# Kernel tuning notes

Measured on AMD Instinct MI355X. Metric: run time of the kernel, lower is better.

The kernel has to match this reference:

```python
import jax, jax.numpy as jnp
import numpy as np

NEG_SLOPE = 0.2  # LeakyReLU negative slope (act_negative)


def setup_inputs() -> dict:
    key = jax.random.key(0)
    ks = jax.random.split(key, 5)
    B, N, D = 64, 4096, 16
    x = jax.random.normal(ks[0], (B, N, D), dtype=jnp.float32)
    # random adjacency, scaled so row sums are O(1) and activations stay stable
    adj = jax.random.uniform(ks[1], (N, N), dtype=jnp.float32) * (2.0 / N)
    Identity = jnp.eye(N, dtype=jnp.float32)
    W0 = jax.random.normal(ks[2], (D, D), dtype=jnp.float32) * (1.0 / np.sqrt(D))
    W1 = jax.random.normal(ks[3], (D, D), dtype=jnp.float32) * (1.0 / np.sqrt(D))
    W2 = jax.random.normal(ks[4], (D, D), dtype=jnp.float32) * (1.0 / np.sqrt(D))
    return {"x": x, "adj": adj, "Identity": Identity, "W0": W0, "W1": W1, "W2": W2}


def _gcn_layer(x, W, adj, I):
    # GCNConv: linear (no bias) -> leaky_relu -> batched adjacency matmul.
    # The same conv (same W) is applied with adj and with Identity, then summed.
    h = jax.nn.leaky_relu(jnp.einsum('bnd,de->bne', x, W), NEG_SLOPE)
    out_adj = jnp.einsum('nm,bmh->bnh', adj, h)  # replaces per-sample torch.mm loop
    out_id = jnp.einsum('nm,bmh->bnh', I, h)
    return out_adj + out_id


def reference(x, adj, Identity, W0, W1, W2):
    out = _gcn_layer(x, W0, adj, Identity)
    out = _gcn_layer(out, W1, adj, Identity)
    out = _gcn_layer(out, W2, adj, Identity)
    return out  # is_residual=False: no shortcut branch
```

## Files before the change

### kernel.cpp

```cpp
#include <hip/hip_runtime.h>
#include <stdint.h>


typedef float  f32x4  __attribute__((ext_vector_type(4)));
typedef unsigned short ushort8 __attribute__((ext_vector_type(8)));
typedef int    i32x4  __attribute__((ext_vector_type(4)));
typedef int    i32x8  __attribute__((ext_vector_type(8)));

typedef __attribute__((address_space(1))) void* as1p;
typedef __attribute__((address_space(3))) void* as3p;
#define GLOAD_LDS16(G, L) \
  __builtin_amdgcn_global_load_lds((as1p)(G), (as3p)(L), 16, 0, 0)

#define P_ELEMS 4194304
#define ADJ_SCALE 4096.0f
#define ADJ_DESCALE (1.0f / 4096.0f)
#define SCALE_ONE 0x7f7f7f7f

__device__ __forceinline__ unsigned short f2bf(float f) {
  unsigned u = __float_as_uint(f);
  u += 0x7fffu + ((u >> 16) & 1u);
  return (unsigned short)(u >> 16);
}
__device__ __forceinline__ float bf2f(unsigned short u) {
  return __uint_as_float(((unsigned)u) << 16);
}
__device__ __forceinline__ int pk4_fp8(float a, float b, float c, float d) {
  int v = __builtin_amdgcn_cvt_pk_fp8_f32(a, b, 0, false);
  v = __builtin_amdgcn_cvt_pk_fp8_f32(c, d, v, true);
  return v;
}

__global__ void prep(const float* __restrict__ adj,
                     unsigned char* __restrict__ a8,
                     const float* __restrict__ x,
                     const float* __restrict__ W,
                     unsigned char* __restrict__ hb8,
                     unsigned short* __restrict__ hnc_out) {
  __shared__ float xs[64 * 65];
  __shared__ unsigned short ht[64 * 72];
  int bid = blockIdx.x;

  if (bid >= 1024) {
    size_t base = ((size_t)(bid - 1024) * 256 + threadIdx.x) * 16;
    const float4* src = (const float4*)(adj + base);
    float4 q0 = src[0], q1 = src[1], q2 = src[2], q3 = src[3];
    int4 o;
    o.x = pk4_fp8(q0.x * ADJ_SCALE, q0.y * ADJ_SCALE, q0.z * ADJ_SCALE, q0.w * ADJ_SCALE);
    o.y = pk4_fp8(q1.x * ADJ_SCALE, q1.y * ADJ_SCALE, q1.z * ADJ_SCALE, q1.w * ADJ_SCALE);
    o.z = pk4_fp8(q2.x * ADJ_SCALE, q2.y * ADJ_SCALE, q2.z * ADJ_SCALE, q2.w * ADJ_SCALE);
    o.w = pk4_fp8(q3.x * ADJ_SCALE, q3.y * ADJ_SCALE, q3.z * ADJ_SCALE, q3.w * ADJ_SCALE);
    *(int4*)(a8 + base) = o;
    return;
  }

  int n0 = (bid & 63) * 64, c0 = (bid >> 6) * 64;

  for (int i = threadIdx.x; i < 1024; i += 256) {
    int bs = i >> 8, rem = i & 255, nr = rem >> 2, d4 = rem & 3;
    float4 v = *(const float4*)(
        x + ((size_t)(c0 / 16 + bs) * 4096 + n0 + nr) * 16 + d4 * 4);
    float* dst = xs + nr * 65 + bs * 16 + d4 * 4;
    dst[0] = v.x; dst[1] = v.y; dst[2] = v.z; dst[3] = v.w;
  }
  __syncthreads();

  int n_l = threadIdx.x & 63, b_l = threadIdx.x >> 6;
  float xv[16];
#pragma unroll
  for (int d = 0; d < 16; ++d) xv[d] = xs[n_l * 65 + b_l * 16 + d];
  float accv[16];
#pragma unroll
  for (int e = 0; e < 16; ++e) accv[e] = 0.f;
#pragma unroll
  for (int d = 0; d < 16; ++d)
#pragma unroll
    for (int e = 0; e < 16; ++e) accv[e] += xv[d] * W[d * 16 + e];

  ushort8 h0, h1;
#pragma unroll
  for (int e = 0; e < 16; ++e) {
    float a = accv[e] > 0.f ? accv[e] : 0.2f * accv[e];
    unsigned short hv = f2bf(a);
    ht[(b_l * 16 + e) * 72 + n_l] = hv;
    if (e < 8) h0[e] = hv; else h1[e - 8] = hv;
  }
  unsigned short* ho = hnc_out + (size_t)(n0 + n_l) * 1024 + c0 + b_l * 16;
  *(ushort8*)(ho)     = h0;
  *(ushort8*)(ho + 8) = h1;
  __syncthreads();

  for (int i = threadIdx.x; i < 512; i += 256) {
    int row = i >> 3, ch = i & 7;
    const unsigned short* s = ht + row * 72 + ch * 8;
    int2 v;
    v.x = pk4_fp8(bf2f(s[0]), bf2f(s[1]), bf2f(s[2]), bf2f(s[3]));
    v.y = pk4_fp8(bf2f(s[4]), bf2f(s[5]), bf2f(s[6]), bf2f(s[7]));
    *(int2*)(hb8 + (size_t)(c0 + row) * 4096 + n0 + ch * 8) = v;
  }
}

__global__ void linear_fuse(const unsigned short* __restrict__ pp,
                            const unsigned short* __restrict__ hnc_in,
                            const float* __restrict__ W,
                            unsigned char* __restrict__ hb8,
                            unsigned short* __restrict__ hnc_out) {
  __shared__ float xs[64 * 65];
  __shared__ unsigned short ht[64 * 72];
  int n0 = blockIdx.x * 64, c0 = blockIdx.y * 64;

  for (int i = threadIdx.x; i < 512; i += 256) {
    int row = i >> 3, ch = i & 7;
    size_t g = (size_t)(n0 + row) * 1024 + c0 + ch * 8;
    ushort8 a = *(const ushort8*)(pp + g);
    ushort8 b = *(const ushort8*)(pp + P_ELEMS + g);
    ushort8 c = *(const ushort8*)(hnc_in + g);
    float* dst = xs + row * 65 + ch * 8;
#pragma unroll
    for (int j = 0; j < 8; ++j) dst[j] = bf2f(a[j]) + bf2f(b[j]) + bf2f(c[j]);
  }
  __syncthreads();

  int n_l = threadIdx.x & 63, b_l = threadIdx.x >> 6;
  float xv[16];
#pragma unroll
  for (int d = 0; d < 16; ++d) xv[d] = xs[n_l * 65 + b_l * 16 + d];
  float accv[16];
#pragma unroll
  for (int e = 0; e < 16; ++e) accv[e] = 0.f;
#pragma unroll
  for (int d = 0; d < 16; ++d)
#pragma unroll
    for (int e = 0; e < 16; ++e) accv[e] += xv[d] * W[d * 16 + e];

  ushort8 h0, h1;
#pragma unroll
  for (int e = 0; e < 16; ++e) {
    float a = accv[e] > 0.f ? accv[e] : 0.2f * accv[e];
    unsigned short hv = f2bf(a);
    ht[(b_l * 16 + e) * 72 + n_l] = hv;
    if (e < 8) h0[e] = hv; else h1[e - 8] = hv;
  }
  unsigned short* ho = hnc_out + (size_t)(n0 + n_l) * 1024 + c0 + b_l * 16;
  *(ushort8*)(ho)     = h0;
  *(ushort8*)(ho + 8) = h1;
  __syncthreads();

  for (int i = threadIdx.x; i < 512; i += 256) {
    int row = i >> 3, ch = i & 7;
    const unsigned short* s = ht + row * 72 + ch * 8;
    int2 v;
    v.x = pk4_fp8(bf2f(s[0]), bf2f(s[1]), bf2f(s[2]), bf2f(s[3]));
    v.y = pk4_fp8(bf2f(s[4]), bf2f(s[5]), bf2f(s[6]), bf2f(s[7]));
    *(int2*)(hb8 + (size_t)(c0 + row) * 4096 + n0 + ch * 8) = v;
  }
}

__global__ void add_out(const unsigned short* __restrict__ pp,
                        const unsigned short* __restrict__ hnc,
                        float* __restrict__ out) {
  int gid = blockIdx.x * 256 + threadIdx.x;
  int n = gid >> 7, c8 = (gid & 127) * 8;
  size_t g = (size_t)n * 1024 + c8;
  ushort8 a = *(const ushort8*)(pp + g);
  ushort8 b = *(const ushort8*)(pp + P_ELEMS + g);
  ushort8 h = *(const ushort8*)(hnc + g);
  float v[8];
#pragma unroll
  for (int j = 0; j < 8; ++j) v[j] = bf2f(a[j]) + bf2f(b[j]) + bf2f(h[j]);
  int bb = c8 >> 4, d0 = c8 & 15;
  float* o = out + (size_t)bb * 65536 + n * 16 + d0;
  *(float4*)(o)     = float4{v[0], v[1], v[2], v[3]};
  *(float4*)(o + 4) = float4{v[4], v[5], v[6], v[7]};
}

__global__ __launch_bounds__(256, 2)
void gemm_f8(const unsigned char* __restrict__ A,
             const unsigned char* __restrict__ B8,
             unsigned short* __restrict__ pp) {
  const int K = 4096;
  __shared__ unsigned char a_s[2][128 * 128];
  __shared__ unsigned char b_s[2][128 * 128];

  int tid = threadIdx.x, wave = tid >> 6, lane = tid & 63;

  int lin = blockIdx.x;
  int xcd = lin & 7, g = lin >> 3;
  int mth = g & 3, ct = (g >> 2) & 7, ks = g >> 5;
  int mt = mth * 8 + xcd;
  int n0 = mt * 128, c0 = ct * 128;
  int kbase = ks * 2048;

  int l8 = lane >> 3, lc = lane & 7;
  int swc = lc ^ l8;
  const unsigned char* gA[4];
  const unsigned char* gB[4];
#pragma unroll
  for (int j = 0; j < 4; ++j) {
    int r = wave * 32 + j * 8 + l8;
    gA[j] = A  + (size_t)(n0 + r) * K + kbase + swc * 16;
    gB[j] = B8 + (size_t)(c0 + r) * K + kbase + swc * 16;
  }

  int i16 = lane & 15, q = lane >> 4;
  int wm = wave >> 1, wn = wave & 1;
  int sw7 = i16 & 7;
  int pc0 = ((2 * q) ^ sw7) * 16;
  int pc1 = ((2 * q + 1) ^ sw7) * 16;

#define STAGE(buf, k0)                                                \
  do {                                                                \
    _Pragma("unroll")                                                 \
    for (int j = 0; j < 4; ++j) {                                     \
      GLOAD_LDS16(gA[j] + (k0), a_s[buf] + (wave * 32 + j * 8) * 128);\
      GLOAD_LDS16(gB[j] + (k0), b_s[buf] + (wave * 32 + j * 8) * 128);\
    }                                                                 \
  } while (0)

#define COMPUTE(buf)                                                  \
  do {                                                                \
    i32x8 bv[4];                                                      \
    _Pragma("unroll")                                                 \
    for (int u = 0; u < 4; ++u) {                                     \
      const unsigned char* bp = b_s[buf] + (wn * 64 + u * 16 + i16) * 128; \
      i32x4 blo = *(const i32x4*)(bp + pc0);                          \
      i32x4 bhi = *(const i32x4*)(bp + pc1);                          \
      bv[u] = __builtin_shufflevector(blo, bhi, 0, 1, 2, 3, 4, 5, 6, 7); \
    }                                                                 \
    _Pragma("unroll")                                                 \
    for (int t = 0; t < 4; ++t) {                                     \
      const unsigned char* ap = a_s[buf] + (wm * 64 + t * 16 + i16) * 128; \
      i32x4 alo = *(const i32x4*)(ap + pc0);                          \
      i32x4 ahi = *(const i32x4*)(ap + pc1);                          \
      i32x8 av = __builtin_shufflevector(alo, ahi, 0, 1, 2, 3, 4, 5, 6, 7); \
      _Pragma("unroll")                                               \
      for (int u = 0; u < 4; ++u)                                     \
        acc[t][u] = __builtin_amdgcn_mfma_scale_f32_16x16x128_f8f6f4( \
            av, bv[u], acc[t][u], 0, 0, 0, SCALE_ONE, 0, SCALE_ONE);  \
    }                                                                 \
  } while (0)

  f32x4 acc[4][4] = {};

  STAGE(0, 0);
  __syncthreads();

  for (int it = 0; it < 16; it += 2) {
    STAGE(1, (it + 1) * 128);
    COMPUTE(0);
    __syncthreads();

    if (it + 2 < 16) STAGE(0, (it + 2) * 128);
    COMPUTE(1);
    __syncthreads();
  }

#undef STAGE
#undef COMPUTE

  unsigned short* dst = pp + (size_t)ks * P_ELEMS;
#pragma unroll
  for (int t = 0; t < 4; ++t)
#pragma unroll
    for (int u = 0; u < 4; ++u)
#pragma unroll
      for (int i = 0; i < 4; ++i) {
        int n_g = n0 + wm * 64 + t * 16 + q * 4 + i;
        int c_g = c0 + wn * 64 + u * 16 + i16;
        dst[(size_t)n_g * 1024 + c_g] = f2bf(acc[t][u][i] * ADJ_DESCALE);
      }
}

extern "C" void kernel_launch(void* const* d_in, const int* in_sizes, int n_in,
                              void* d_out, int out_size, void* d_ws, size_t ws_size,
                              hipStream_t stream) {
  const float* x   = (const float*)d_in[0];
  const float* adj = (const float*)d_in[1];
  const float* W0  = (const float*)d_in[3];
  const float* W1  = (const float*)d_in[4];
  const float* W2  = (const float*)d_in[5];
  float* out = (float*)d_out;

  char* ws = (char*)d_ws;
  unsigned char*  adj8 = (unsigned char*)ws;
  unsigned char*  hb8  = (unsigned char*)(ws + 16777216);
  unsigned short* hnc  = (unsigned short*)(ws + 20971520);
  unsigned short* pp   = (unsigned short*)(ws + 29360128);

  prep<<<5120, 256, 0, stream>>>(adj, adj8, x, W0, hb8, hnc);
  gemm_f8<<<512, 256, 0, stream>>>(adj8, hb8, pp);
  linear_fuse<<<dim3(64, 16), 256, 0, stream>>>(pp, hnc, W1, hb8, hnc);
  gemm_f8<<<512, 256, 0, stream>>>(adj8, hb8, pp);
  linear_fuse<<<dim3(64, 16), 256, 0, stream>>>(pp, hnc, W2, hb8, hnc);
  gemm_f8<<<512, 256, 0, stream>>>(adj8, hb8, pp);
  add_out<<<2048, 256, 0, stream>>>(pp, hnc, out);
}
```

Baseline: 246.9 us.

## Fuse linear+activation epilogue into FP8 GEMM, drop split-K, triple-buffer LDS

Removes the split-K partial buffers and the separate linear_fuse/add_out kernels by doing the full K reduction in one block and running the residual add, 16x16 linear, LeakyReLU and FP8 transposed repack in the GEMM epilogue through LDS. The main loop moves to a three-stage global_load_lds pipeline with explicit vmcnt waits and barriers, and occupancy is lowered to one block per CU. This saves the partial-sum write/read traffic and kernel launches but halves the grid to 256 blocks with a longer K loop, which risks underfilling the CUs. Ping-pong hb8 buffers avoid read/write hazards across layers.

Measured after the change: 261.7 us. 1.06x slower.

```diff
diff --git a/kernel.cpp b/kernel.cpp
--- a/kernel.cpp
+++ b/kernel.cpp
@@ -12,7 +12,6 @@
 #define GLOAD_LDS16(G, L) \
   __builtin_amdgcn_global_load_lds((as1p)(G), (as3p)(L), 16, 0, 0)
 
-#define P_ELEMS 4194304
 #define ADJ_SCALE 4096.0f
 #define ADJ_DESCALE (1.0f / 4096.0f)
 #define SCALE_ONE 0x7f7f7f7f
@@ -100,96 +99,26 @@
   }
 }
 
-__global__ void linear_fuse(const unsigned short* __restrict__ pp,
-                            const unsigned short* __restrict__ hnc_in,
-                            const float* __restrict__ W,
-                            unsigned char* __restrict__ hb8,
-                            unsigned short* __restrict__ hnc_out) {
-  __shared__ float xs[64 * 65];
-  __shared__ unsigned short ht[64 * 72];
-  int n0 = blockIdx.x * 64, c0 = blockIdx.y * 64;
-
-  for (int i = threadIdx.x; i < 512; i += 256) {
-    int row = i >> 3, ch = i & 7;
-    size_t g = (size_t)(n0 + row) * 1024 + c0 + ch * 8;
-    ushort8 a = *(const ushort8*)(pp + g);
-    ushort8 b = *(const ushort8*)(pp + P_ELEMS + g);
-    ushort8 c = *(const ushort8*)(hnc_in + g);
-    float* dst = xs + row * 65 + ch * 8;
-#pragma unroll
-    for (int j = 0; j < 8; ++j) dst[j] = bf2f(a[j]) + bf2f(b[j]) + bf2f(c[j]);
-  }
-  __syncthreads();
-
-  int n_l = threadIdx.x & 63, b_l = threadIdx.x >> 6;
-  float xv[16];
-#pragma unroll
-  for (int d = 0; d < 16; ++d) xv[d] = xs[n_l * 65 + b_l * 16 + d];
-  float accv[16];
-#pragma unroll
-  for (int e = 0; e < 16; ++e) accv[e] = 0.f;
-#pragma unroll
-  for (int d = 0; d < 16; ++d)
-#pragma unroll
-    for (int e = 0; e < 16; ++e) accv[e] += xv[d] * W[d * 16 + e];
-
-  ushort8 h0, h1;
-#pragma unroll
-  for (int e = 0; e < 16; ++e) {
-    float a = accv[e] > 0.f ? accv[e] : 0.2f * accv[e];
-    unsigned short hv = f2bf(a);
-    ht[(b_l * 16 + e) * 72 + n_l] = hv;
-    if (e < 8) h0[e] = hv; else h1[e - 8] = hv;
-  }
-  unsigned short* ho = hnc_out + (size_t)(n0 + n_l) * 1024 + c0 + b_l * 16;
-  *(ushort8*)(ho)     = h0;
-  *(ushort8*)(ho + 8) = h1;
-  __syncthreads();
-
-  for (int i = threadIdx.x; i < 512; i += 256) {
-    int row = i >> 3, ch = i & 7;
-    const unsigned short* s = ht + row * 72 + ch * 8;
-    int2 v;
-    v.x = pk4_fp8(bf2f(s[0]), bf2f(s[1]), bf2f(s[2]), bf2f(s[3]));
-    v.y = pk4_fp8(bf2f(s[4]), bf2f(s[5]), bf2f(s[6]), bf2f(s[7]));
-    *(int2*)(hb8 + (size_t)(c0 + row) * 4096 + n0 + ch * 8) = v;
-  }
-}
-
-__global__ void add_out(const unsigned short* __restrict__ pp,
-                        const unsigned short* __restrict__ hnc,
-                        float* __restrict__ out) {
-  int gid = blockIdx.x * 256 + threadIdx.x;
-  int n = gid >> 7, c8 = (gid & 127) * 8;
-  size_t g = (size_t)n * 1024 + c8;
-  ushort8 a = *(const ushort8*)(pp + g);
-  ushort8 b = *(const ushort8*)(pp + P_ELEMS + g);
-  ushort8 h = *(const ushort8*)(hnc + g);
-  float v[8];
-#pragma unroll
-  for (int j = 0; j < 8; ++j) v[j] = bf2f(a[j]) + bf2f(b[j]) + bf2f(h[j]);
-  int bb = c8 >> 4, d0 = c8 & 15;
-  float* o = out + (size_t)bb * 65536 + n * 16 + d0;
-  *(float4*)(o)     = float4{v[0], v[1], v[2], v[3]};
-  *(float4*)(o + 4) = float4{v[4], v[5], v[6], v[7]};
-}
-
-__global__ __launch_bounds__(256, 2)
+__global__ __launch_bounds__(256, 1)
 void gemm_f8(const unsigned char* __restrict__ A,
              const unsigned char* __restrict__ B8,
-             unsigned short* __restrict__ pp) {
+             const float* __restrict__ Wn,
+             unsigned short* __restrict__ hnc,
+             unsigned char* __restrict__ hb8o,
+             float* __restrict__ out,
+             int mode) {
   const int K = 4096;
-  __shared__ unsigned char a_s[2][128 * 128];
-  __shared__ unsigned char b_s[2][128 * 128];
+  __shared__ unsigned char smem[98304];
+  unsigned char* a_s[3] = {smem, smem + 16384, smem + 32768};
+  unsigned char* b_s[3] = {smem + 49152, smem + 65536, smem + 81920};
 
   int tid = threadIdx.x, wave = tid >> 6, lane = tid & 63;
 
   int lin = blockIdx.x;
   int xcd = lin & 7, g = lin >> 3;
-  int mth = g & 3, ct = (g >> 2) & 7, ks = g >> 5;
+  int mth = g & 3, ct = g >> 2;
   int mt = mth * 8 + xcd;
   int n0 = mt * 128, c0 = ct * 128;
-  int kbase = ks * 2048;
 
   int l8 = lane >> 3, lc = lane & 7;
   int swc = lc ^ l8;
@@ -198,8 +127,8 @@
 #pragma unroll
   for (int j = 0; j < 4; ++j) {
     int r = wave * 32 + j * 8 + l8;
-    gA[j] = A  + (size_t)(n0 + r) * K + kbase + swc * 16;
-    gB[j] = B8 + (size_t)(c0 + r) * K + kbase + swc * 16;
+    gA[j] = A  + (size_t)(n0 + r) * K + swc * 16;
+    gB[j] = B8 + (size_t)(c0 + r) * K + swc * 16;
   }
 
   int i16 = lane & 15, q = lane >> 4;
@@ -208,12 +137,13 @@
   int pc0 = ((2 * q) ^ sw7) * 16;
   int pc1 = ((2 * q + 1) ^ sw7) * 16;
 
-#define STAGE(buf, k0)                                                \
+#define STAGE(buf, it)                                                \
   do {                                                                \
+    int k0_ = (it) * 128;                                             \
     _Pragma("unroll")                                                 \
     for (int j = 0; j < 4; ++j) {                                     \
-      GLOAD_LDS16(gA[j] + (k0), a_s[buf] + (wave * 32 + j * 8) * 128);\
-      GLOAD_LDS16(gB[j] + (k0), b_s[buf] + (wave * 32 + j * 8) * 128);\
+      GLOAD_LDS16(gA[j] + k0_, a_s[buf] + (wave * 32 + j * 8) * 128); \
+      GLOAD_LDS16(gB[j] + k0_, b_s[buf] + (wave * 32 + j * 8) * 128); \
     }                                                                 \
   } while (0)
 
@@ -240,35 +170,113 @@
     }                                                                 \
   } while (0)
 
+#define WAITVM8() asm volatile("s_waitcnt vmcnt(8)" ::: "memory")
+#define WAITVM0() asm volatile("s_waitcnt vmcnt(0)" ::: "memory")
+#define BARX() do { __builtin_amdgcn_s_barrier(); \
+                    asm volatile("" ::: "memory"); } while (0)
+
   f32x4 acc[4][4] = {};
 
   STAGE(0, 0);
-  __syncthreads();
-
-  for (int it = 0; it < 16; it += 2) {
-    STAGE(1, (it + 1) * 128);
-    COMPUTE(0);
-    __syncthreads();
-
-    if (it + 2 < 16) STAGE(0, (it + 2) * 128);
-    COMPUTE(1);
-    __syncthreads();
-  }
+  STAGE(1, 1);
+
+  for (int itb = 0; itb < 30; itb += 3) {
+    WAITVM8(); BARX(); STAGE(2, itb + 2); COMPUTE(0);
+    WAITVM8(); BARX(); STAGE(0, itb + 3); COMPUTE(1);
+    WAITVM8(); BARX(); STAGE(1, itb + 4); COMPUTE(2);
+  }
+  WAITVM8(); BARX(); COMPUTE(0);
+  WAITVM0(); BARX(); COMPUTE(1);
 
 #undef STAGE
 #undef COMPUTE
-
-  unsigned short* dst = pp + (size_t)ks * P_ELEMS;
+#undef WAITVM8
+#undef WAITVM0
+#undef BARX
+
+  __syncthreads();
+  float* u_lds = (float*)smem;
+  unsigned short* ht = (unsigned short*)(smem + 65536);
+
 #pragma unroll
   for (int t = 0; t < 4; ++t)
 #pragma unroll
     for (int u = 0; u < 4; ++u)
 #pragma unroll
       for (int i = 0; i < 4; ++i) {
-        int n_g = n0 + wm * 64 + t * 16 + q * 4 + i;
-        int c_g = c0 + wn * 64 + u * 16 + i16;
-        dst[(size_t)n_g * 1024 + c_g] = f2bf(acc[t][u][i] * ADJ_DESCALE);
+        int n_l = wm * 64 + t * 16 + q * 4 + i;
+        int c_l = wn * 64 + u * 16 + i16;
+        u_lds[n_l * 128 + (c_l ^ (((n_l >> 2) & 1) << 4))] = acc[t][u][i];
       }
+  __syncthreads();
+
+  if (mode == 0) {
+    for (int s = 0; s < 4; ++s) {
+      int item = s * 256 + tid;
+      int n_l = item & 127, gi = item >> 7;
+      int pg = gi ^ ((n_l >> 2) & 1);
+      const float* up = u_lds + n_l * 128 + pg * 16;
+      size_t gb = (size_t)(n0 + n_l) * 1024 + c0 + gi * 16;
+      ushort8 hn0 = *(const ushort8*)(hnc + gb);
+      ushort8 hn1 = *(const ushort8*)(hnc + gb + 8);
+      float ud[16];
+#pragma unroll
+      for (int d = 0; d < 8; ++d) {
+        ud[d]     = up[d]     * ADJ_DESCALE + bf2f(hn0[d]);
+        ud[d + 8] = up[d + 8] * ADJ_DESCALE + bf2f(hn1[d]);
+      }
+      float hv[16];
+#pragma unroll
+      for (int e = 0; e < 16; ++e) hv[e] = 0.f;
+#pragma unroll
+      for (int d = 0; d < 16; ++d)
+#pragma unroll
+        for (int e = 0; e < 16; ++e) hv[e] += ud[d] * Wn[d * 16 + e];
+      ushort8 o0, o1;
+#pragma unroll
+      for (int e = 0; e < 16; ++e) {
+        float a = hv[e] > 0.f ? hv[e] : 0.2f * hv[e];
+        unsigned short hb = f2bf(a);
+        if (e < 8) o0[e] = hb; else o1[e - 8] = hb;
+        int cr = gi * 16 + e;
+        ht[cr * 128 + (((n_l >> 3) ^ (cr & 15)) << 3) + (n_l & 7)] = hb;
+      }
+      *(ushort8*)(hnc + gb)     = o0;
+      *(ushort8*)(hnc + gb + 8) = o1;
+    }
+    __syncthreads();
+    for (int s = 0; s < 8; ++s) {
+      int item = s * 256 + tid;
+      int c_l = item >> 4, n8 = item & 15;
+      const unsigned short* hp = ht + c_l * 128 + ((n8 ^ (c_l & 15)) << 3);
+      int2 v;
+      v.x = pk4_fp8(bf2f(hp[0]), bf2f(hp[1]), bf2f(hp[2]), bf2f(hp[3]));
+      v.y = pk4_fp8(bf2f(hp[4]), bf2f(hp[5]), bf2f(hp[6]), bf2f(hp[7]));
+      *(int2*)(hb8o + (size_t)(c0 + c_l) * 4096 + n0 + n8 * 8) = v;
+    }
+  } else {
+    for (int s = 0; s < 4; ++s) {
+      int item = s * 256 + tid;
+      int n_l = item & 127, gi = item >> 7;
+      int pg = gi ^ ((n_l >> 2) & 1);
+      const float* up = u_lds + n_l * 128 + pg * 16;
+      size_t gb = (size_t)(n0 + n_l) * 1024 + c0 + gi * 16;
+      ushort8 hn0 = *(const ushort8*)(hnc + gb);
+      ushort8 hn1 = *(const ushort8*)(hnc + gb + 8);
+      float v[16];
+#pragma unroll
+      for (int d = 0; d < 8; ++d) {
+        v[d]     = up[d]     * ADJ_DESCALE + bf2f(hn0[d]);
+        v[d + 8] = up[d + 8] * ADJ_DESCALE + bf2f(hn1[d]);
+      }
+      int bb = (c0 >> 4) + gi;
+      float* op = out + (size_t)bb * 65536 + (size_t)(n0 + n_l) * 16;
+      *(float4*)(op)      = float4{v[0],  v[1],  v[2],  v[3]};
+      *(float4*)(op + 4)  = float4{v[4],  v[5],  v[6],  v[7]};
+      *(float4*)(op + 8)  = float4{v[8],  v[9],  v[10], v[11]};
+      *(float4*)(op + 12) = float4{v[12], v[13], v[14], v[15]};
+    }
+  }
 }
 
 extern "C" void kernel_launch(void* const* d_in, const int* in_sizes, int n_in,
@@ -282,16 +290,14 @@
   float* out = (float*)d_out;
 
   char* ws = (char*)d_ws;
-  unsigned char*  adj8 = (unsigned char*)ws;
-  unsigned char*  hb8  = (unsigned char*)(ws + 16777216);
-  unsigned short* hnc  = (unsigned short*)(ws + 20971520);
-  unsigned short* pp   = (unsigned short*)(ws + 29360128);
-
-  prep<<<5120, 256, 0, stream>>>(adj, adj8, x, W0, hb8, hnc);
-  gemm_f8<<<512, 256, 0, stream>>>(adj8, hb8, pp);
-  linear_fuse<<<dim3(64, 16), 256, 0, stream>>>(pp, hnc, W1, hb8, hnc);
-  gemm_f8<<<512, 256, 0, stream>>>(adj8, hb8, pp);
-  linear_fuse<<<dim3(64, 16), 256, 0, stream>>>(pp, hnc, W2, hb8, hnc);
-  gemm_f8<<<512, 256, 0, stream>>>(adj8, hb8, pp);
-  add_out<<<2048, 256, 0, stream>>>(pp, hnc, out);
-}
+  unsigned char*  adj8  = (unsigned char*)ws;
+  unsigned char*  hb8_a = (unsigned char*)(ws + 16777216);
+  unsigned char*  hb8_b = (unsigned char*)(ws + 20971520);
+  unsigned short* hnc   = (unsigned short*)(ws + 25165824);
+
+  prep<<<5120, 256, 0, stream>>>(adj, adj8, x, W0, hb8_a, hnc);
+  gemm_f8<<<256, 256, 0, stream>>>(adj8, hb8_a, W1, hnc, hb8_b, out, 0);
+  gemm_f8<<<256, 256, 0, stream>>>(adj8, hb8_b, W2, hnc, hb8_a, out, 0);
+  gemm_f8<<<256, 256, 0, stream>>>(adj8, hb8_a, (const float*)nullptr,
+                                   hnc, (unsigned char*)nullptr, out, 1);
+}
```

## Deepen FP8 GEMM prefetch with vmcnt-based waits and MFMA priority boost

Applied to the files above, without the earlier changes.

The double-buffered K loop now issues two stages ahead and replaces full __syncthreads with a partial s_waitcnt vmcnt(8) plus raw barriers. This lets the next tile's global-to-LDS loads stay in flight while the current tile computes. It also raises wave priority around the MFMA block via s_setprio so that math issue is favored. The hand-written waitcnt counting must exactly match the 8 loads per stage, or buffers get read before they are ready.

Result: no change. 246.8 us (-0.0%).

```diff
diff --git a/kernel.cpp b/kernel.cpp
--- a/kernel.cpp
+++ b/kernel.cpp
@@ -208,12 +208,13 @@
   int pc0 = ((2 * q) ^ sw7) * 16;
   int pc1 = ((2 * q + 1) ^ sw7) * 16;
 
-#define STAGE(buf, k0)                                                \
+#define STAGE(buf, it)                                                \
   do {                                                                \
+    int k0_ = (it) * 128;                                             \
     _Pragma("unroll")                                                 \
     for (int j = 0; j < 4; ++j) {                                     \
-      GLOAD_LDS16(gA[j] + (k0), a_s[buf] + (wave * 32 + j * 8) * 128);\
-      GLOAD_LDS16(gB[j] + (k0), b_s[buf] + (wave * 32 + j * 8) * 128);\
+      GLOAD_LDS16(gA[j] + k0_, a_s[buf] + (wave * 32 + j * 8) * 128); \
+      GLOAD_LDS16(gB[j] + k0_, b_s[buf] + (wave * 32 + j * 8) * 128); \
     }                                                                 \
   } while (0)
 
@@ -227,6 +228,7 @@
       i32x4 bhi = *(const i32x4*)(bp + pc1);                          \
       bv[u] = __builtin_shufflevector(blo, bhi, 0, 1, 2, 3, 4, 5, 6, 7); \
     }                                                                 \
+    __builtin_amdgcn_s_setprio(1);                                    \
     _Pragma("unroll")                                                 \
     for (int t = 0; t < 4; ++t) {                                     \
       const unsigned char* ap = a_s[buf] + (wm * 64 + t * 16 + i16) * 128; \
@@ -238,25 +240,32 @@
         acc[t][u] = __builtin_amdgcn_mfma_scale_f32_16x16x128_f8f6f4( \
             av, bv[u], acc[t][u], 0, 0, 0, SCALE_ONE, 0, SCALE_ONE);  \
     }                                                                 \
+    __builtin_amdgcn_s_setprio(0);                                    \
   } while (0)
 
+#define WAITVM8() asm volatile("s_waitcnt vmcnt(8)" ::: "memory")
+#define WAITVM0() asm volatile("s_waitcnt vmcnt(0)" ::: "memory")
+#define BARX() do { asm volatile("" ::: "memory");                    \
+                    __builtin_amdgcn_s_barrier();                     \
+                    asm volatile("" ::: "memory"); } while (0)
+
   f32x4 acc[4][4] = {};
 
   STAGE(0, 0);
-  __syncthreads();
-
-  for (int it = 0; it < 16; it += 2) {
-    STAGE(1, (it + 1) * 128);
-    COMPUTE(0);
-    __syncthreads();
-
-    if (it + 2 < 16) STAGE(0, (it + 2) * 128);
-    COMPUTE(1);
-    __syncthreads();
-  }
+  STAGE(1, 1);
+
+  for (int itb = 0; itb < 14; itb += 2) {
+    WAITVM8(); BARX(); COMPUTE(0); BARX(); STAGE(0, itb + 2);
+    WAITVM8(); BARX(); COMPUTE(1); BARX(); STAGE(1, itb + 3);
+  }
+  WAITVM8(); BARX(); COMPUTE(0);
+  WAITVM0(); BARX(); COMPUTE(1);
 
 #undef STAGE
 #undef COMPUTE
+#undef WAITVM8
+#undef WAITVM0
+#undef BARX
 
   unsigned short* dst = pp + (size_t)ks * P_ELEMS;
 #pragma unroll
```

## Replace double-buffered K=128 staging with single-buffer K=256 tiles and MFMA priority

Applied to the files above, without the earlier changes.

The GEMM main loop drops the two-buffer ping-pong over 128-wide K slices. It now uses a single LDS buffer holding 256-wide K slices, loaded and then consumed with a barrier on each side. This halves the number of loop iterations and barriers and raises priority around the MFMA block via s_setprio. The cost is that global loads no longer overlap compute within a block, so the design relies on the two co-resident blocks per CU to hide latency. The load address and swizzle mapping is rewritten to fit 256-byte rows.

After: 245.7 us. About the same (-0.5%).

```diff
diff --git a/kernel.cpp b/kernel.cpp
--- a/kernel.cpp
+++ b/kernel.cpp
@@ -179,8 +179,8 @@
              const unsigned char* __restrict__ B8,
              unsigned short* __restrict__ pp) {
   const int K = 4096;
-  __shared__ unsigned char a_s[2][128 * 128];
-  __shared__ unsigned char b_s[2][128 * 128];
+  __shared__ unsigned char a_s[128 * 256];
+  __shared__ unsigned char b_s[128 * 256];
 
   int tid = threadIdx.x, wave = tid >> 6, lane = tid & 63;
 
@@ -191,16 +191,16 @@
   int n0 = mt * 128, c0 = ct * 128;
   int kbase = ks * 2048;
 
-  int l8 = lane >> 3, lc = lane & 7;
-  int swc = lc ^ l8;
-  const unsigned char* gA[4];
-  const unsigned char* gB[4];
-#pragma unroll
-  for (int j = 0; j < 4; ++j) {
-    int r = wave * 32 + j * 8 + l8;
-    gA[j] = A  + (size_t)(n0 + r) * K + kbase + swc * 16;
-    gB[j] = B8 + (size_t)(c0 + r) * K + kbase + swc * 16;
-  }
+  int l16 = lane >> 4, p15 = lane & 15;
+  int half = p15 >> 3, pc7 = p15 & 7;
+  int ko0 = (half * 8 + (pc7 ^ l16)) * 16;
+  int ko1 = (half * 8 + (pc7 ^ (4 + l16))) * 16;
+  const unsigned char* pA[2];
+  const unsigned char* pB[2];
+  pA[0] = A  + (size_t)(n0 + wave * 32 + l16) * K + kbase + ko0;
+  pA[1] = A  + (size_t)(n0 + wave * 32 + 4 + l16) * K + kbase + ko1;
+  pB[0] = B8 + (size_t)(c0 + wave * 32 + l16) * K + kbase + ko0;
+  pB[1] = B8 + (size_t)(c0 + wave * 32 + 4 + l16) * K + kbase + ko1;
 
   int i16 = lane & 15, q = lane >> 4;
   int wm = wave >> 1, wn = wave & 1;
@@ -208,50 +208,56 @@
   int pc0 = ((2 * q) ^ sw7) * 16;
   int pc1 = ((2 * q + 1) ^ sw7) * 16;
 
-#define STAGE(buf, k0)                                                \
+#define STAGE(it)                                                     \
+  do {                                                                \
+    int k0_ = (it) * 256;                                             \
+    _Pragma("unroll")                                                 \
+    for (int j = 0; j < 8; ++j) {                                     \
+      GLOAD_LDS16(pA[j & 1] + (size_t)(j >> 1) * 8 * K + k0_,         \
+                  a_s + wave * 8192 + j * 1024);                      \
+      GLOAD_LDS16(pB[j & 1] + (size_t)(j >> 1) * 8 * K + k0_,         \
+                  b_s + wave * 8192 + j * 1024);                      \
+    }                                                                 \
+  } while (0)
+
+#define COMPUTE()                                                     \
   do {                                                                \
     _Pragma("unroll")                                                 \
-    for (int j = 0; j < 4; ++j) {                                     \
-      GLOAD_LDS16(gA[j] + (k0), a_s[buf] + (wave * 32 + j * 8) * 128);\
-      GLOAD_LDS16(gB[j] + (k0), b_s[buf] + (wave * 32 + j * 8) * 128);\
+    for (int s01 = 0; s01 < 2; ++s01) {                               \
+      int sb = s01 * 128;                                             \
+      i32x8 bv[4];                                                    \
+      _Pragma("unroll")                                               \
+      for (int u = 0; u < 4; ++u) {                                   \
+        const unsigned char* bp =                                     \
+            b_s + (wn * 64 + u * 16 + i16) * 256 + sb;                \
+        i32x4 blo = *(const i32x4*)(bp + pc0);                        \
+        i32x4 bhi = *(const i32x4*)(bp + pc1);                        \
+        bv[u] = __builtin_shufflevector(blo, bhi, 0, 1, 2, 3, 4, 5, 6, 7); \
+      }                                                               \
+      __builtin_amdgcn_s_setprio(1);                                  \
+      _Pragma("unroll")                                               \
+      for (int t = 0; t < 4; ++t) {                                   \
+        const unsigned char* ap =                                     \
+            a_s + (wm * 64 + t * 16 + i16) * 256 + sb;                \
+        i32x4 alo = *(const i32x4*)(ap + pc0);                        \
+        i32x4 ahi = *(const i32x4*)(ap + pc1);                        \
+        i32x8 av = __builtin_shufflevector(alo, ahi, 0, 1, 2, 3, 4, 5, 6, 7); \
+        _Pragma("unroll")                                             \
+        for (int u = 0; u < 4; ++u)                                   \
+          acc[t][u] = __builtin_amdgcn_mfma_scale_f32_16x16x128_f8f6f4( \
+              av, bv[u], acc[t][u], 0, 0, 0, SCALE_ONE, 0, SCALE_ONE);  \
+      }                                                               \
+      __builtin_amdgcn_s_setprio(0);                                  \
     }                                                                 \
   } while (0)
 
-#define COMPUTE(buf)                                                  \
-  do {                                                                \
-    i32x8 bv[4];                                                      \
-    _Pragma("unroll")                                                 \
-    for (int u = 0; u < 4; ++u) {                                     \
-      const unsigned char* bp = b_s[buf] + (wn * 64 + u * 16 + i16) * 128; \
-      i32x4 blo = *(const i32x4*)(bp + pc0);                          \
-      i32x4 bhi = *(const i32x4*)(bp + pc1);                          \
-      bv[u] = __builtin_shufflevector(blo, bhi, 0, 1, 2, 3, 4, 5, 6, 7); \
-    }                                                                 \
-    _Pragma("unroll")                                                 \
-    for (int t = 0; t < 4; ++t) {                                     \
-      const unsigned char* ap = a_s[buf] + (wm * 64 + t * 16 + i16) * 128; \
-      i32x4 alo = *(const i32x4*)(ap + pc0);                          \
-      i32x4 ahi = *(const i32x4*)(ap + pc1);                          \
-      i32x8 av = __builtin_shufflevector(alo, ahi, 0, 1, 2, 3, 4, 5, 6, 7); \
-      _Pragma("unroll")                                               \
-      for (int u = 0; u < 4; ++u)                                     \
-        acc[t][u] = __builtin_amdgcn_mfma_scale_f32_16x16x128_f8f6f4( \
-            av, bv[u], acc[t][u], 0, 0, 0, SCALE_ONE, 0, SCALE_ONE);  \
-    }                                                                 \
-  } while (0)
-
   f32x4 acc[4][4] = {};
 
-  STAGE(0, 0);
-  __syncthreads();
-
-  for (int it = 0; it < 16; it += 2) {
-    STAGE(1, (it + 1) * 128);
-    COMPUTE(0);
+#pragma unroll 1
+  for (int it = 0; it < 8; ++it) {
+    STAGE(it);
     __syncthreads();
-
-    if (it + 2 < 16) STAGE(0, (it + 2) * 128);
-    COMPUTE(1);
+    COMPUTE();
     __syncthreads();
   }
 
```
